# Performance work log

Hardware: AMD Instinct MI355X
Metric: run time of the kernel (lower is better)

## Reference

```python
import jax, jax.numpy as jnp
import numpy as np

NUM_BINS = 64
Z_MIN, Z_MAX = -3.0, 1.0
BIN_SIZE = (Z_MAX - Z_MIN) / NUM_BINS
EPS_MEAN = 1e-5
EPS_BN = 1e-5


def setup_inputs() -> dict:
    key = jax.random.key(0)
    k1, k2, k3, k4 = jax.random.split(key, 4)
    M, N, C = 100000, 64, 4
    feat_channels, out_dim = 64, NUM_BINS * 3
    features = jax.random.normal(k1, (M, N, C), dtype=jnp.float32)
    num_points = jax.random.randint(k2, (M,), 0, 65, dtype=jnp.int32)
    coors = jax.random.randint(k3, (M, 4), 0, 100, dtype=jnp.int32)
    W = jax.random.normal(k4, (feat_channels, out_dim), dtype=jnp.float32) * (1.0 / np.sqrt(out_dim))
    b = jnp.zeros((feat_channels,), dtype=jnp.float32)
    gamma = jnp.ones((feat_channels,), dtype=jnp.float32)
    beta = jnp.zeros((feat_channels,), dtype=jnp.float32)
    return {"features": features, "num_points": num_points, "coors": coors,
            "W": W, "b": b, "gamma": gamma, "beta": beta}


def reference(features, num_points, coors, W, b, gamma, beta):
    M, N, C = features.shape
    # validity mask per point
    mask = (jnp.arange(N)[None, :] < num_points[:, None]).astype(features.dtype)  # [M, N]
    z = features[..., 2]  # [M, N]
    r = features[..., 3]  # [M, N]
    bin_idx = jnp.clip(((z - Z_MIN) / BIN_SIZE).astype(jnp.int32), 0, NUM_BINS - 1)  # [M, N]

    rows = jnp.arange(M)[:, None]  # [M, 1] broadcast against [M, N]
    zeros = jnp.zeros((M, NUM_BINS), dtype=features.dtype)
    count = zeros.at[rows, bin_idx].add(mask)
    sum_z = zeros.at[rows, bin_idx].add(z * mask)
    sum_r = zeros.at[rows, bin_idx].add(r * mask)
    mean_z = sum_z / (count + EPS_MEAN)
    mean_r = sum_r / (count + EPS_MEAN)

    # interleaved layout [count, mean_z, mean_r] per bin -> [M, 3*NUM_BINS]
    hist = jnp.stack([count, mean_z, mean_r], axis=-1).reshape(M, NUM_BINS * 3)

    # Linear -> BatchNorm1d (training: biased batch stats) -> ReLU
    x = hist @ W.T + b  # [M, feat_channels]
    mu = jnp.mean(x, axis=0)
    var = jnp.mean((x - mu) ** 2, axis=0)
    xn = (x - mu) / jnp.sqrt(var + EPS_BN)
    return jax.nn.relu(xn * gamma + beta)
```

## Files before the change

### kernel.cpp

```cpp
#include <hip/hip_runtime.h>
#include <hip/hip_bf16.h>
#include <math.h>


typedef __attribute__((ext_vector_type(8))) short bf16x8;
typedef __attribute__((ext_vector_type(4))) float f32x4;
typedef __attribute__((ext_vector_type(4))) int   i32x4;

#define ZMINF   (-3.0f)
#define INV_BIN 16.0f
#define QS      8192.0f
#define INV_QS  (1.0f / 8192.0f)
#define PBIASF  65536.0f
#define PBIASI  65536
#define CBIT    16777216
#define TSC     16777216.0f
#define INV_TSC (1.0f / 16777216.0f)
#define REPS    16
#define RSTRIDE 66

__device__ __forceinline__ short f2bf(float f) {
    __hip_bfloat16 h = __float2bfloat16(f);
    return __builtin_bit_cast(short, h);
}

__global__ __launch_bounds__(256)
void k0_prep(const float* __restrict__ W,
             short*       __restrict__ wsW,
             unsigned long long* __restrict__ totals)
{
    const int tid    = blockIdx.x * 256 + threadIdx.x;
    const int stride = gridDim.x * 256;
    for (int e = tid; e < 24 * 64 * 8; e += stride) {
        const int j  = e & 7;
        const int ln = (e >> 3) & 63;
        const int st = e >> 9;
        const int s  = st >> 2, t = st & 3;
        const int k  = s * 32 + (ln >> 4) * 8 + j;
        const int n  = t * 16 + (ln & 15);
        const int wc = (k < 64) ? 3 * k
                     : (k < 128) ? 3 * (k - 64) + 1
                                 : 3 * (k - 128) + 2;
        wsW[e] = f2bf(W[n * 192 + wc]);
    }
    for (int e = tid; e < REPS * 128; e += stride) totals[e] = 0ull;
}

__global__ __launch_bounds__(128, 8)
void k1_hist_mfma(const uint2*  __restrict__ feat2,
                  const int*    __restrict__ nump,
                  const bf16x8* __restrict__ wsWf,
                  const float*  __restrict__ bvec,
                  float*        __restrict__ xout,
                  unsigned long long* __restrict__ totals,
                  int M)
{
    __shared__ unsigned long long sH[16 * RSTRIDE];

    const int tid  = threadIdx.x;
    const int wave = tid >> 6;
    const int lane = tid & 63;
    const int col  = lane & 15;
    const int quad = lane >> 4;
    const int half = wave;

    const int gbase = blockIdx.x * 16;
    float psum[2] = {0.f, 0.f};
    float psq[2]  = {0.f, 0.f};
    bf16x8 bcur[2];

    if (gbase < M) {
        uint2 zw[8];
        const int npv = nump[min(gbase + half * 8 + (lane & 7), M - 1)];
        #pragma unroll
        for (int uu = 0; uu < 8; ++uu) {
            const int rc = min(gbase + half * 8 + uu, M - 1);
            zw[uu] = feat2[((size_t)rc * 64 + lane) * 2 + 1];
        }

        {
            i32x4* p4 = (i32x4*)&sH[(size_t)half * 8 * RSTRIDE];
            #pragma unroll
            for (int i = 0; i < 5; ++i) {
                const int idx = lane + i * 64;
                if (idx < (8 * RSTRIDE * 2) / 4) p4[idx] = i32x4{0, 0, 0, 0};
            }
        }
        __builtin_amdgcn_wave_barrier();

        #pragma unroll
        for (int uu = 0; uu < 8; ++uu) {
            const int u = half * 8 + uu;
            int np_u = __builtin_amdgcn_readlane(npv, uu);
            np_u = (gbase + u < M) ? np_u : 0;
            if (lane < np_u) {
                const float z  = __int_as_float((int)zw[uu].x);
                const float rr = __int_as_float((int)zw[uu].y);
                int bi = (int)((z - ZMINF) * INV_BIN);
                bi = min(max(bi, 0), 63);
                const unsigned long long add =
                    ((unsigned long long)(unsigned)(CBIT + PBIASI + (int)(z * QS)) << 32)
                    | (unsigned)(PBIASI + (int)(rr * QS));
                atomicAdd(&sH[u * RSTRIDE + bi], add);
            }
        }

        bcur[0] = wsWf[(half * 2 + 0) * 64 + lane];
        bcur[1] = wsWf[(half * 2 + 1) * 64 + lane];
    }

    __syncthreads();

    if (gbase < M) {
        f32x4 acc[2] = {};
        bf16x8 bnxt[2];
        const int* ar = (const int*)sH + col * (RSTRIDE * 2);
        #pragma unroll
        for (int g = 0; g < 2; ++g) {
            const int o0 = g * 32 + quad * 8;
            const i32x4* ap = (const i32x4*)(ar + 2 * o0);
            const i32x4 a0 = ap[0], a1 = ap[1], a2 = ap[2], a3 = ap[3];
            const int zz[8]  = {a0.y, a0.w, a1.y, a1.w, a2.y, a2.w, a3.y, a3.w};
            const int rrw[8] = {a0.x, a0.z, a1.x, a1.z, a2.x, a2.z, a3.x, a3.z};
            float cnt[8], rcp[8], av[8];
            bf16x8 af;

            bnxt[0] = wsWf[((2 + g) * 4 + half * 2 + 0) * 64 + lane];
            bnxt[1] = wsWf[((2 + g) * 4 + half * 2 + 1) * 64 + lane];
            #pragma unroll
            for (int j = 0; j < 8; ++j) { cnt[j] = (float)(zz[j] >> 24); av[j] = cnt[j]; }
            #pragma unroll
            for (int j = 0; j < 8; ++j) af[j] = f2bf(av[j]);
            acc[0] = __builtin_amdgcn_mfma_f32_16x16x32_bf16(af, bcur[0], acc[0], 0, 0, 0);
            acc[1] = __builtin_amdgcn_mfma_f32_16x16x32_bf16(af, bcur[1], acc[1], 0, 0, 0);
            bcur[0] = bnxt[0]; bcur[1] = bnxt[1];

            bnxt[0] = wsWf[((4 + g) * 4 + half * 2 + 0) * 64 + lane];
            bnxt[1] = wsWf[((4 + g) * 4 + half * 2 + 1) * 64 + lane];
            #pragma unroll
            for (int j = 0; j < 8; ++j) {
                rcp[j] = __builtin_amdgcn_rcpf(cnt[j] + 1e-5f) * INV_QS;
                const float pay = (float)(zz[j] & 0xFFFFFF);
                av[j] = (pay - cnt[j] * PBIASF) * rcp[j];
            }
            #pragma unroll
            for (int j = 0; j < 8; ++j) af[j] = f2bf(av[j]);
            acc[0] = __builtin_amdgcn_mfma_f32_16x16x32_bf16(af, bcur[0], acc[0], 0, 0, 0);
            acc[1] = __builtin_amdgcn_mfma_f32_16x16x32_bf16(af, bcur[1], acc[1], 0, 0, 0);
            bcur[0] = bnxt[0]; bcur[1] = bnxt[1];

            if (g == 0) {
                bnxt[0] = wsWf[(1 * 4 + half * 2 + 0) * 64 + lane];
                bnxt[1] = wsWf[(1 * 4 + half * 2 + 1) * 64 + lane];
            }
            #pragma unroll
            for (int j = 0; j < 8; ++j)
                av[j] = ((float)rrw[j] - cnt[j] * PBIASF) * rcp[j];
            #pragma unroll
            for (int j = 0; j < 8; ++j) af[j] = f2bf(av[j]);
            acc[0] = __builtin_amdgcn_mfma_f32_16x16x32_bf16(af, bcur[0], acc[0], 0, 0, 0);
            acc[1] = __builtin_amdgcn_mfma_f32_16x16x32_bf16(af, bcur[1], acc[1], 0, 0, 0);
            bcur[0] = bnxt[0]; bcur[1] = bnxt[1];
        }

        #pragma unroll
        for (int tt = 0; tt < 2; ++tt) {
            const int t = half * 2 + tt;
            const float bias = bvec[t * 16 + col];
            #pragma unroll
            for (int i = 0; i < 4; ++i) {
                const int row = gbase + quad * 4 + i;
                if (row < M) {
                    const float xv = acc[tt][i] + bias;
                    xout[(size_t)row * 64 + t * 16 + col] = xv;
                    psum[tt] += xv;
                    psq[tt]  += xv * xv;
                }
            }
        }
    }

    #pragma unroll
    for (int tt = 0; tt < 2; ++tt) {
        psum[tt] += __shfl_xor(psum[tt], 16);
        psum[tt] += __shfl_xor(psum[tt], 32);
        psq[tt]  += __shfl_xor(psq[tt], 16);
        psq[tt]  += __shfl_xor(psq[tt], 32);
    }
    const float myS = (quad & 1) ? psum[1] : psum[0];
    const float myQ = (quad & 1) ? psq[1]  : psq[0];
    const int gw = blockIdx.x * 2 + wave;
    if (lane < 32) {
        unsigned long long* dst = totals + (gw & (REPS - 1)) * 128 + half * 32 + lane;
        atomicAdd(dst,      (unsigned long long)(long long)(myS * TSC));
        atomicAdd(dst + 64, (unsigned long long)(long long)(myQ * TSC));
    }
}

__global__ __launch_bounds__(256)
void k3_bn_apply(float4* __restrict__ x,
                 const unsigned long long* __restrict__ totals,
                 const float* __restrict__ gamma,
                 const float* __restrict__ beta,
                 float invM, int n4)
{
    __shared__ float sT[128];
    __shared__ float sa[64];
    __shared__ float sc[64];
    const int t = threadIdx.x;
    if (t < 128) {
        long long s = 0;
        #pragma unroll
        for (int rep = 0; rep < REPS; ++rep) s += (long long)totals[rep * 128 + t];
        sT[t] = (float)s * (invM * INV_TSC);
    }
    __syncthreads();
    if (t < 64) {
        const float mu   = sT[t];
        const float q    = sT[64 + t];
        const float var  = q - mu * mu;
        const float rstd = 1.0f / sqrtf(var + 1e-5f);
        const float a    = gamma[t] * rstd;
        sa[t] = a;
        sc[t] = beta[t] - mu * a;
    }
    __syncthreads();
    const int stride = gridDim.x * 256;
    for (int i = blockIdx.x * 256 + t; i < n4; i += stride) {
        const float4 a = ((const float4*)sa)[i & 15];
        const float4 c = ((const float4*)sc)[i & 15];
        float4 v = x[i];
        v.x = fmaxf(fmaf(v.x, a.x, c.x), 0.f);
        v.y = fmaxf(fmaf(v.y, a.y, c.y), 0.f);
        v.z = fmaxf(fmaf(v.z, a.z, c.z), 0.f);
        v.w = fmaxf(fmaf(v.w, a.w, c.w), 0.f);
        x[i] = v;
    }
}

extern "C" void kernel_launch(void* const* d_in, const int* in_sizes, int n_in,
                              void* d_out, int out_size, void* d_ws, size_t ws_size,
                              hipStream_t stream) {
    const uint2*  feat2 = (const uint2*)d_in[0];
    const int*    nump  = (const int*)d_in[1];
    const float*  W     = (const float*)d_in[3];
    const float*  bvec  = (const float*)d_in[4];
    const float*  gamma = (const float*)d_in[5];
    const float*  beta  = (const float*)d_in[6];

    const int M = in_sizes[1];
    float* xout = (float*)d_out;
    short* wsW  = (short*)d_ws;
    unsigned long long* totals =
        (unsigned long long*)((char*)d_ws + 24 * 64 * 8 * sizeof(short));

    k0_prep<<<16, 256, 0, stream>>>(W, wsW, totals);

    const int nblk = (M + 15) / 16;
    k1_hist_mfma<<<nblk, 128, 0, stream>>>(feat2, nump, (const bf16x8*)wsW, bvec, xout, totals, M);

    const int n4 = out_size / 4;
    const int nblk3 = (n4 + 256 * 16 - 1) / (256 * 16);
    k3_bn_apply<<<nblk3, 256, 0, stream>>>((float4*)d_out, totals, gamma, beta,
                                           1.0f / (float)M, n4);
}
```

Baseline: 185.0 us.

## Process four tiles per block with double-buffered histogram and prefetched features

Each block now loops over four 16-row tiles, prefetching the next tile's z/r features and point counts into registers while the current tile is histogrammed and multiplied. The LDS histogram is double-buffered so one barrier per tile suffices. All six W fragments are loaded into registers once per block instead of being streamed per tile. The launch-bound occupancy hint drops to raise register budget, and the grid shrinks fourfold, trading parallelism for amortized setup and latency hiding.

```diff
diff --git a/kernel.cpp b/kernel.cpp
--- a/kernel.cpp
+++ b/kernel.cpp
@@ -18,6 +18,7 @@
 #define INV_TSC (1.0f / 16777216.0f)
 #define REPS    16
 #define RSTRIDE 66
+#define TILES   4
 
 __device__ __forceinline__ short f2bf(float f) {
     __hip_bfloat16 h = __float2bfloat16(f);
@@ -46,7 +47,7 @@
     for (int e = tid; e < REPS * 128; e += stride) totals[e] = 0ull;
 }
 
-__global__ __launch_bounds__(128, 8)
+__global__ __launch_bounds__(128, 3)
 void k1_hist_mfma(const uint2*  __restrict__ feat2,
                   const int*    __restrict__ nump,
                   const bf16x8* __restrict__ wsWf,
@@ -55,126 +56,138 @@
                   unsigned long long* __restrict__ totals,
                   int M)
 {
-    __shared__ unsigned long long sH[16 * RSTRIDE];
+    __shared__ unsigned long long sH[2][16 * RSTRIDE];
 
     const int tid  = threadIdx.x;
-    const int wave = tid >> 6;
+    const int half = tid >> 6;
     const int lane = tid & 63;
     const int col  = lane & 15;
     const int quad = lane >> 4;
-    const int half = wave;
-
-    const int gbase = blockIdx.x * 16;
+
+    const int gbase0 = blockIdx.x * (16 * TILES);
+
+    bf16x8 bfr[6][2];
+    #pragma unroll
+    for (int p = 0; p < 6; ++p) {
+        #pragma unroll
+        for (int tt = 0; tt < 2; ++tt)
+            bfr[p][tt] = wsWf[(p * 4 + half * 2 + tt) * 64 + lane];
+    }
+
     float psum[2] = {0.f, 0.f};
     float psq[2]  = {0.f, 0.f};
-    bf16x8 bcur[2];
-
-    if (gbase < M) {
-        uint2 zw[8];
-        const int npv = nump[min(gbase + half * 8 + (lane & 7), M - 1)];
+
+    uint2 zw[2][8];
+    int   npv[2];
+
+    {
+        npv[0] = nump[min(gbase0 + half * 8 + (lane & 7), M - 1)];
         #pragma unroll
         for (int uu = 0; uu < 8; ++uu) {
-            const int rc = min(gbase + half * 8 + uu, M - 1);
-            zw[uu] = feat2[((size_t)rc * 64 + lane) * 2 + 1];
+            const int rc = min(gbase0 + half * 8 + uu, M - 1);
+            zw[0][uu] = feat2[((size_t)rc * 64 + lane) * 2 + 1];
         }
-
-        {
-            i32x4* p4 = (i32x4*)&sH[(size_t)half * 8 * RSTRIDE];
+    }
+
+    #pragma unroll
+    for (int t = 0; t < TILES; ++t) {
+        const int gbase = gbase0 + t * 16;
+        if (gbase < M) {
+            const int cur = t & 1;
+            const int nxt = cur ^ 1;
+
+            if (t + 1 < TILES) {
+                const int gb = gbase0 + (t + 1) * 16;
+                npv[nxt] = nump[min(gb + half * 8 + (lane & 7), M - 1)];
+                #pragma unroll
+                for (int uu = 0; uu < 8; ++uu) {
+                    const int rc = min(gb + half * 8 + uu, M - 1);
+                    zw[nxt][uu] = feat2[((size_t)rc * 64 + lane) * 2 + 1];
+                }
+            }
+
+            {
+                int* base = (int*)&sH[cur][0];
+                #pragma unroll
+                for (int i = 0; i < 4; ++i) {
+                    const int idx = lane + i * 64;
+                    const int off = (half * 8 + (idx >> 5)) * (RSTRIDE * 2) + (idx & 31) * 4;
+                    *(i32x4*)(base + off) = i32x4{0, 0, 0, 0};
+                }
+            }
+            __builtin_amdgcn_wave_barrier();
+
             #pragma unroll
-            for (int i = 0; i < 5; ++i) {
-                const int idx = lane + i * 64;
-                if (idx < (8 * RSTRIDE * 2) / 4) p4[idx] = i32x4{0, 0, 0, 0};
-            }
-        }
-        __builtin_amdgcn_wave_barrier();
-
-        #pragma unroll
-        for (int uu = 0; uu < 8; ++uu) {
-            const int u = half * 8 + uu;
-            int np_u = __builtin_amdgcn_readlane(npv, uu);
-            np_u = (gbase + u < M) ? np_u : 0;
-            if (lane < np_u) {
-                const float z  = __int_as_float((int)zw[uu].x);
-                const float rr = __int_as_float((int)zw[uu].y);
-                int bi = (int)((z - ZMINF) * INV_BIN);
-                bi = min(max(bi, 0), 63);
-                const unsigned long long add =
-                    ((unsigned long long)(unsigned)(CBIT + PBIASI + (int)(z * QS)) << 32)
-                    | (unsigned)(PBIASI + (int)(rr * QS));
-                atomicAdd(&sH[u * RSTRIDE + bi], add);
-            }
-        }
-
-        bcur[0] = wsWf[(half * 2 + 0) * 64 + lane];
-        bcur[1] = wsWf[(half * 2 + 1) * 64 + lane];
-    }
-
-    __syncthreads();
-
-    if (gbase < M) {
-        f32x4 acc[2] = {};
-        bf16x8 bnxt[2];
-        const int* ar = (const int*)sH + col * (RSTRIDE * 2);
-        #pragma unroll
-        for (int g = 0; g < 2; ++g) {
-            const int o0 = g * 32 + quad * 8;
-            const i32x4* ap = (const i32x4*)(ar + 2 * o0);
-            const i32x4 a0 = ap[0], a1 = ap[1], a2 = ap[2], a3 = ap[3];
-            const int zz[8]  = {a0.y, a0.w, a1.y, a1.w, a2.y, a2.w, a3.y, a3.w};
-            const int rrw[8] = {a0.x, a0.z, a1.x, a1.z, a2.x, a2.z, a3.x, a3.z};
-            float cnt[8], rcp[8], av[8];
-            bf16x8 af;
-
-            bnxt[0] = wsWf[((2 + g) * 4 + half * 2 + 0) * 64 + lane];
-            bnxt[1] = wsWf[((2 + g) * 4 + half * 2 + 1) * 64 + lane];
+            for (int uu = 0; uu < 8; ++uu) {
+                const int u = half * 8 + uu;
+                int np_u = __builtin_amdgcn_readlane(npv[cur], uu);
+                np_u = (gbase + u < M) ? np_u : 0;
+                if (lane < np_u) {
+                    const float z  = __int_as_float((int)zw[cur][uu].x);
+                    const float rr = __int_as_float((int)zw[cur][uu].y);
+                    int bi = (int)((z - ZMINF) * INV_BIN);
+                    bi = min(max(bi, 0), 63);
+                    const unsigned long long add =
+                        ((unsigned long long)(unsigned)(CBIT + PBIASI + (int)(z * QS)) << 32)
+                        | (unsigned)(PBIASI + (int)(rr * QS));
+                    atomicAdd(&sH[cur][u * RSTRIDE + bi], add);
+                }
+            }
+
+            __syncthreads();
+
+            f32x4 acc[2] = {};
+            const int* ar = (const int*)&sH[cur][0] + col * (RSTRIDE * 2);
             #pragma unroll
-            for (int j = 0; j < 8; ++j) { cnt[j] = (float)(zz[j] >> 24); av[j] = cnt[j]; }
+            for (int g = 0; g < 2; ++g) {
+                const int o0 = g * 32 + quad * 8;
+                const i32x4* ap = (const i32x4*)(ar + 2 * o0);
+                const i32x4 a0 = ap[0], a1 = ap[1], a2 = ap[2], a3 = ap[3];
+                const int zz[8]  = {a0.y, a0.w, a1.y, a1.w, a2.y, a2.w, a3.y, a3.w};
+                const int rrw[8] = {a0.x, a0.z, a1.x, a1.z, a2.x, a2.z, a3.x, a3.z};
+                float cnt[8], rcp[8], av[8];
+                bf16x8 af;
+
+                #pragma unroll
+                for (int j = 0; j < 8; ++j) { cnt[j] = (float)(zz[j] >> 24); av[j] = cnt[j]; }
+                #pragma unroll
+                for (int j = 0; j < 8; ++j) af[j] = f2bf(av[j]);
+                acc[0] = __builtin_amdgcn_mfma_f32_16x16x32_bf16(af, bfr[g][0], acc[0], 0, 0, 0);
+                acc[1] = __builtin_amdgcn_mfma_f32_16x16x32_bf16(af, bfr[g][1], acc[1], 0, 0, 0);
+
+                #pragma unroll
+                for (int j = 0; j < 8; ++j) {
+                    rcp[j] = __builtin_amdgcn_rcpf(cnt[j] + 1e-5f) * INV_QS;
+                    const float pay = (float)(zz[j] & 0xFFFFFF);
+                    av[j] = (pay - cnt[j] * PBIASF) * rcp[j];
+                }
+                #pragma unroll
+                for (int j = 0; j < 8; ++j) af[j] = f2bf(av[j]);
+                acc[0] = __builtin_amdgcn_mfma_f32_16x16x32_bf16(af, bfr[2 + g][0], acc[0], 0, 0, 0);
+                acc[1] = __builtin_amdgcn_mfma_f32_16x16x32_bf16(af, bfr[2 + g][1], acc[1], 0, 0, 0);
+
+                #pragma unroll
+                for (int j = 0; j < 8; ++j)
+                    av[j] = ((float)rrw[j] - cnt[j] * PBIASF) * rcp[j];
+                #pragma unroll
+                for (int j = 0; j < 8; ++j) af[j] = f2bf(av[j]);
+                acc[0] = __builtin_amdgcn_mfma_f32_16x16x32_bf16(af, bfr[4 + g][0], acc[0], 0, 0, 0);
+                acc[1] = __builtin_amdgcn_mfma_f32_16x16x32_bf16(af, bfr[4 + g][1], acc[1], 0, 0, 0);
+            }
+
             #pragma unroll
-            for (int j = 0; j < 8; ++j) af[j] = f2bf(av[j]);
-            acc[0] = __builtin_amdgcn_mfma_f32_16x16x32_bf16(af, bcur[0], acc[0], 0, 0, 0);
-            acc[1] = __builtin_amdgcn_mfma_f32_16x16x32_bf16(af, bcur[1], acc[1], 0, 0, 0);
-            bcur[0] = bnxt[0]; bcur[1] = bnxt[1];
-
-            bnxt[0] = wsWf[((4 + g) * 4 + half * 2 + 0) * 64 + lane];
-            bnxt[1] = wsWf[((4 + g) * 4 + half * 2 + 1) * 64 + lane];
-            #pragma unroll
-            for (int j = 0; j < 8; ++j) {
-                rcp[j] = __builtin_amdgcn_rcpf(cnt[j] + 1e-5f) * INV_QS;
-                const float pay = (float)(zz[j] & 0xFFFFFF);
-                av[j] = (pay - cnt[j] * PBIASF) * rcp[j];
-            }
-            #pragma unroll
-            for (int j = 0; j < 8; ++j) af[j] = f2bf(av[j]);
-            acc[0] = __builtin_amdgcn_mfma_f32_16x16x32_bf16(af, bcur[0], acc[0], 0, 0, 0);
-            acc[1] = __builtin_amdgcn_mfma_f32_16x16x32_bf16(af, bcur[1], acc[1], 0, 0, 0);
-            bcur[0] = bnxt[0]; bcur[1] = bnxt[1];
-
-            if (g == 0) {
-                bnxt[0] = wsWf[(1 * 4 + half * 2 + 0) * 64 + lane];
-                bnxt[1] = wsWf[(1 * 4 + half * 2 + 1) * 64 + lane];
-            }
-            #pragma unroll
-            for (int j = 0; j < 8; ++j)
-                av[j] = ((float)rrw[j] - cnt[j] * PBIASF) * rcp[j];
-            #pragma unroll
-            for (int j = 0; j < 8; ++j) af[j] = f2bf(av[j]);
-            acc[0] = __builtin_amdgcn_mfma_f32_16x16x32_bf16(af, bcur[0], acc[0], 0, 0, 0);
-            acc[1] = __builtin_amdgcn_mfma_f32_16x16x32_bf16(af, bcur[1], acc[1], 0, 0, 0);
-            bcur[0] = bnxt[0]; bcur[1] = bnxt[1];
-        }
-
-        #pragma unroll
-        for (int tt = 0; tt < 2; ++tt) {
-            const int t = half * 2 + tt;
-            const float bias = bvec[t * 16 + col];
-            #pragma unroll
-            for (int i = 0; i < 4; ++i) {
-                const int row = gbase + quad * 4 + i;
-                if (row < M) {
-                    const float xv = acc[tt][i] + bias;
-                    xout[(size_t)row * 64 + t * 16 + col] = xv;
-                    psum[tt] += xv;
-                    psq[tt]  += xv * xv;
+            for (int tt = 0; tt < 2; ++tt) {
+                const int tch = half * 2 + tt;
+                const float bias = bvec[tch * 16 + col];
+                #pragma unroll
+                for (int i = 0; i < 4; ++i) {
+                    const int row = gbase + quad * 4 + i;
+                    if (row < M) {
+                        const float xv = acc[tt][i] + bias;
+                        xout[(size_t)row * 64 + tch * 16 + col] = xv;
+                        psum[tt] += xv;
+                        psq[tt]  += xv * xv;
+                    }
                 }
             }
         }
@@ -189,9 +202,8 @@
     }
     const float myS = (quad & 1) ? psum[1] : psum[0];
     const float myQ = (quad & 1) ? psq[1]  : psq[0];
-    const int gw = blockIdx.x * 2 + wave;
     if (lane < 32) {
-        unsigned long long* dst = totals + (gw & (REPS - 1)) * 128 + half * 32 + lane;
+        unsigned long long* dst = totals + (blockIdx.x & (REPS - 1)) * 128 + half * 32 + lane;
         atomicAdd(dst,      (unsigned long long)(long long)(myS * TSC));
         atomicAdd(dst + 64, (unsigned long long)(long long)(myQ * TSC));
     }
@@ -256,7 +268,7 @@
 
     k0_prep<<<16, 256, 0, stream>>>(W, wsW, totals);
 
-    const int nblk = (M + 15) / 16;
+    const int nblk = (M + 16 * TILES - 1) / (16 * TILES);
     k1_hist_mfma<<<nblk, 128, 0, stream>>>(feat2, nump, (const bf16x8*)wsW, bvec, xout, totals, M);
 
     const int n4 = out_size / 4;
```

New measurement: 190.1 us. 1.03x slower.

## Process two voxel tiles per block with software-prefetched feature loads

Applied to the files above, without the earlier changes.

Each block now handles two 16-voxel tiles in sequence. The feature and point-count loads for the next tile are issued before the current tile's MFMA stage runs, so global load latency overlaps with compute. Bias loads and the BN-stat atomics are amortized over more rows, and the grid is halved. In exchange, register use grows because two tiles of feature buffers are live at once, so the occupancy hint drops from 8 to 6 blocks per CU, and an extra block barrier is needed between tiles.

```diff
diff --git a/kernel.cpp b/kernel.cpp
--- a/kernel.cpp
+++ b/kernel.cpp
@@ -18,6 +18,7 @@
 #define INV_TSC (1.0f / 16777216.0f)
 #define REPS    16
 #define RSTRIDE 66
+#define TILES   2
 
 __device__ __forceinline__ short f2bf(float f) {
     __hip_bfloat16 h = __float2bfloat16(f);
@@ -46,7 +47,7 @@
     for (int e = tid; e < REPS * 128; e += stride) totals[e] = 0ull;
 }
 
-__global__ __launch_bounds__(128, 8)
+__global__ __launch_bounds__(128, 6)
 void k1_hist_mfma(const uint2*  __restrict__ feat2,
                   const int*    __restrict__ nump,
                   const bf16x8* __restrict__ wsWf,
@@ -58,125 +59,147 @@
     __shared__ unsigned long long sH[16 * RSTRIDE];
 
     const int tid  = threadIdx.x;
-    const int wave = tid >> 6;
+    const int half = tid >> 6;
     const int lane = tid & 63;
     const int col  = lane & 15;
     const int quad = lane >> 4;
-    const int half = wave;
-
-    const int gbase = blockIdx.x * 16;
+
+    const int gbase0 = blockIdx.x * (16 * TILES);
+
     float psum[2] = {0.f, 0.f};
     float psq[2]  = {0.f, 0.f};
-    bf16x8 bcur[2];
-
-    if (gbase < M) {
-        uint2 zw[8];
-        const int npv = nump[min(gbase + half * 8 + (lane & 7), M - 1)];
+
+    const float bias0 = bvec[(half * 2 + 0) * 16 + col];
+    const float bias1 = bvec[(half * 2 + 1) * 16 + col];
+
+    uint2 zw[2][8];
+    int   npv[2];
+
+    {
+        npv[0] = nump[min(gbase0 + half * 8 + (lane & 7), M - 1)];
         #pragma unroll
         for (int uu = 0; uu < 8; ++uu) {
-            const int rc = min(gbase + half * 8 + uu, M - 1);
-            zw[uu] = feat2[((size_t)rc * 64 + lane) * 2 + 1];
+            const int rc = min(gbase0 + half * 8 + uu, M - 1);
+            zw[0][uu] = feat2[((size_t)rc * 64 + lane) * 2 + 1];
         }
-
-        {
-            i32x4* p4 = (i32x4*)&sH[(size_t)half * 8 * RSTRIDE];
+    }
+
+    #pragma unroll
+    for (int t = 0; t < TILES; ++t) {
+        const int gbase = gbase0 + t * 16;
+        if (gbase < M) {
+            const int cur = t & 1;
+            const int nxt = cur ^ 1;
+
+            {
+                i32x4* p4 = (i32x4*)&sH[(size_t)half * 8 * RSTRIDE];
+                #pragma unroll
+                for (int i = 0; i < 5; ++i) {
+                    const int idx = lane + i * 64;
+                    if (idx < (8 * RSTRIDE * 2) / 4) p4[idx] = i32x4{0, 0, 0, 0};
+                }
+            }
+            __builtin_amdgcn_wave_barrier();
+
             #pragma unroll
-            for (int i = 0; i < 5; ++i) {
-                const int idx = lane + i * 64;
-                if (idx < (8 * RSTRIDE * 2) / 4) p4[idx] = i32x4{0, 0, 0, 0};
-            }
-        }
-        __builtin_amdgcn_wave_barrier();
-
-        #pragma unroll
-        for (int uu = 0; uu < 8; ++uu) {
-            const int u = half * 8 + uu;
-            int np_u = __builtin_amdgcn_readlane(npv, uu);
-            np_u = (gbase + u < M) ? np_u : 0;
-            if (lane < np_u) {
-                const float z  = __int_as_float((int)zw[uu].x);
-                const float rr = __int_as_float((int)zw[uu].y);
-                int bi = (int)((z - ZMINF) * INV_BIN);
-                bi = min(max(bi, 0), 63);
-                const unsigned long long add =
-                    ((unsigned long long)(unsigned)(CBIT + PBIASI + (int)(z * QS)) << 32)
-                    | (unsigned)(PBIASI + (int)(rr * QS));
-                atomicAdd(&sH[u * RSTRIDE + bi], add);
-            }
-        }
-
-        bcur[0] = wsWf[(half * 2 + 0) * 64 + lane];
-        bcur[1] = wsWf[(half * 2 + 1) * 64 + lane];
-    }
-
-    __syncthreads();
-
-    if (gbase < M) {
-        f32x4 acc[2] = {};
-        bf16x8 bnxt[2];
-        const int* ar = (const int*)sH + col * (RSTRIDE * 2);
-        #pragma unroll
-        for (int g = 0; g < 2; ++g) {
-            const int o0 = g * 32 + quad * 8;
-            const i32x4* ap = (const i32x4*)(ar + 2 * o0);
-            const i32x4 a0 = ap[0], a1 = ap[1], a2 = ap[2], a3 = ap[3];
-            const int zz[8]  = {a0.y, a0.w, a1.y, a1.w, a2.y, a2.w, a3.y, a3.w};
-            const int rrw[8] = {a0.x, a0.z, a1.x, a1.z, a2.x, a2.z, a3.x, a3.z};
-            float cnt[8], rcp[8], av[8];
-            bf16x8 af;
-
-            bnxt[0] = wsWf[((2 + g) * 4 + half * 2 + 0) * 64 + lane];
-            bnxt[1] = wsWf[((2 + g) * 4 + half * 2 + 1) * 64 + lane];
+            for (int uu = 0; uu < 8; ++uu) {
+                const int u = half * 8 + uu;
+                int np_u = __builtin_amdgcn_readlane(npv[cur], uu);
+                np_u = (gbase + u < M) ? np_u : 0;
+                if (lane < np_u) {
+                    const float z  = __int_as_float((int)zw[cur][uu].x);
+                    const float rr = __int_as_float((int)zw[cur][uu].y);
+                    int bi = (int)((z - ZMINF) * INV_BIN);
+                    bi = min(max(bi, 0), 63);
+                    const unsigned long long add =
+                        ((unsigned long long)(unsigned)(CBIT + PBIASI + (int)(z * QS)) << 32)
+                        | (unsigned)(PBIASI + (int)(rr * QS));
+                    atomicAdd(&sH[u * RSTRIDE + bi], add);
+                }
+            }
+
+            if (t + 1 < TILES) {
+                const int gb = gbase0 + (t + 1) * 16;
+                npv[nxt] = nump[min(gb + half * 8 + (lane & 7), M - 1)];
+                #pragma unroll
+                for (int uu = 0; uu < 8; ++uu) {
+                    const int rc = min(gb + half * 8 + uu, M - 1);
+                    zw[nxt][uu] = feat2[((size_t)rc * 64 + lane) * 2 + 1];
+                }
+            }
+
+            bf16x8 bcur[2], bnxt[2];
+            bcur[0] = wsWf[(half * 2 + 0) * 64 + lane];
+            bcur[1] = wsWf[(half * 2 + 1) * 64 + lane];
+
+            __syncthreads();
+
+            f32x4 acc[2] = {};
+            const int* ar = (const int*)sH + col * (RSTRIDE * 2);
             #pragma unroll
-            for (int j = 0; j < 8; ++j) { cnt[j] = (float)(zz[j] >> 24); av[j] = cnt[j]; }
-            #pragma unroll
-            for (int j = 0; j < 8; ++j) af[j] = f2bf(av[j]);
-            acc[0] = __builtin_amdgcn_mfma_f32_16x16x32_bf16(af, bcur[0], acc[0], 0, 0, 0);
-            acc[1] = __builtin_amdgcn_mfma_f32_16x16x32_bf16(af, bcur[1], acc[1], 0, 0, 0);
-            bcur[0] = bnxt[0]; bcur[1] = bnxt[1];
-
-            bnxt[0] = wsWf[((4 + g) * 4 + half * 2 + 0) * 64 + lane];
-            bnxt[1] = wsWf[((4 + g) * 4 + half * 2 + 1) * 64 + lane];
-            #pragma unroll
-            for (int j = 0; j < 8; ++j) {
-                rcp[j] = __builtin_amdgcn_rcpf(cnt[j] + 1e-5f) * INV_QS;
-                const float pay = (float)(zz[j] & 0xFFFFFF);
-                av[j] = (pay - cnt[j] * PBIASF) * rcp[j];
-            }
-            #pragma unroll
-            for (int j = 0; j < 8; ++j) af[j] = f2bf(av[j]);
-            acc[0] = __builtin_amdgcn_mfma_f32_16x16x32_bf16(af, bcur[0], acc[0], 0, 0, 0);
-            acc[1] = __builtin_amdgcn_mfma_f32_16x16x32_bf16(af, bcur[1], acc[1], 0, 0, 0);
-            bcur[0] = bnxt[0]; bcur[1] = bnxt[1];
-
-            if (g == 0) {
-                bnxt[0] = wsWf[(1 * 4 + half * 2 + 0) * 64 + lane];
-                bnxt[1] = wsWf[(1 * 4 + half * 2 + 1) * 64 + lane];
-            }
-            #pragma unroll
-            for (int j = 0; j < 8; ++j)
-                av[j] = ((float)rrw[j] - cnt[j] * PBIASF) * rcp[j];
-            #pragma unroll
-            for (int j = 0; j < 8; ++j) af[j] = f2bf(av[j]);
-            acc[0] = __builtin_amdgcn_mfma_f32_16x16x32_bf16(af, bcur[0], acc[0], 0, 0, 0);
-            acc[1] = __builtin_amdgcn_mfma_f32_16x16x32_bf16(af, bcur[1], acc[1], 0, 0, 0);
-            bcur[0] = bnxt[0]; bcur[1] = bnxt[1];
-        }
-
-        #pragma unroll
-        for (int tt = 0; tt < 2; ++tt) {
-            const int t = half * 2 + tt;
-            const float bias = bvec[t * 16 + col];
+            for (int g = 0; g < 2; ++g) {
+                const int o0 = g * 32 + quad * 8;
+                const i32x4* ap = (const i32x4*)(ar + 2 * o0);
+                const i32x4 a0 = ap[0], a1 = ap[1], a2 = ap[2], a3 = ap[3];
+                const int zz[8]  = {a0.y, a0.w, a1.y, a1.w, a2.y, a2.w, a3.y, a3.w};
+                const int rrw[8] = {a0.x, a0.z, a1.x, a1.z, a2.x, a2.z, a3.x, a3.z};
+                float cnt[8], rcp[8], av[8];
+                bf16x8 af;
+
+                bnxt[0] = wsWf[((2 + g) * 4 + half * 2 + 0) * 64 + lane];
+                bnxt[1] = wsWf[((2 + g) * 4 + half * 2 + 1) * 64 + lane];
+                #pragma unroll
+                for (int j = 0; j < 8; ++j) { cnt[j] = (float)(zz[j] >> 24); av[j] = cnt[j]; }
+                #pragma unroll
+                for (int j = 0; j < 8; ++j) af[j] = f2bf(av[j]);
+                acc[0] = __builtin_amdgcn_mfma_f32_16x16x32_bf16(af, bcur[0], acc[0], 0, 0, 0);
+                acc[1] = __builtin_amdgcn_mfma_f32_16x16x32_bf16(af, bcur[1], acc[1], 0, 0, 0);
+                bcur[0] = bnxt[0]; bcur[1] = bnxt[1];
+
+                bnxt[0] = wsWf[((4 + g) * 4 + half * 2 + 0) * 64 + lane];
+                bnxt[1] = wsWf[((4 + g) * 4 + half * 2 + 1) * 64 + lane];
+                #pragma unroll
+                for (int j = 0; j < 8; ++j) {
+                    rcp[j] = __builtin_amdgcn_rcpf(cnt[j] + 1e-5f) * INV_QS;
+                    const float pay = (float)(zz[j] & 0xFFFFFF);
+                    av[j] = (pay - cnt[j] * PBIASF) * rcp[j];
+                }
+                #pragma unroll
+                for (int j = 0; j < 8; ++j) af[j] = f2bf(av[j]);
+                acc[0] = __builtin_amdgcn_mfma_f32_16x16x32_bf16(af, bcur[0], acc[0], 0, 0, 0);
+                acc[1] = __builtin_amdgcn_mfma_f32_16x16x32_bf16(af, bcur[1], acc[1], 0, 0, 0);
+                bcur[0] = bnxt[0]; bcur[1] = bnxt[1];
+
+                if (g == 0) {
+                    bnxt[0] = wsWf[(1 * 4 + half * 2 + 0) * 64 + lane];
+                    bnxt[1] = wsWf[(1 * 4 + half * 2 + 1) * 64 + lane];
+                }
+                #pragma unroll
+                for (int j = 0; j < 8; ++j)
+                    av[j] = ((float)rrw[j] - cnt[j] * PBIASF) * rcp[j];
+                #pragma unroll
+                for (int j = 0; j < 8; ++j) af[j] = f2bf(av[j]);
+                acc[0] = __builtin_amdgcn_mfma_f32_16x16x32_bf16(af, bcur[0], acc[0], 0, 0, 0);
+                acc[1] = __builtin_amdgcn_mfma_f32_16x16x32_bf16(af, bcur[1], acc[1], 0, 0, 0);
+                bcur[0] = bnxt[0]; bcur[1] = bnxt[1];
+            }
+
             #pragma unroll
             for (int i = 0; i < 4; ++i) {
                 const int row = gbase + quad * 4 + i;
                 if (row < M) {
-                    const float xv = acc[tt][i] + bias;
-                    xout[(size_t)row * 64 + t * 16 + col] = xv;
-                    psum[tt] += xv;
-                    psq[tt]  += xv * xv;
-                }
-            }
+                    const float xv0 = acc[0][i] + bias0;
+                    const float xv1 = acc[1][i] + bias1;
+                    float* xr = xout + (size_t)row * 64 + half * 32 + col;
+                    xr[0]  = xv0;
+                    xr[16] = xv1;
+                    psum[0] += xv0; psq[0] += xv0 * xv0;
+                    psum[1] += xv1; psq[1] += xv1 * xv1;
+                }
+            }
+
+            if (t + 1 < TILES)
+                __syncthreads();
         }
     }
 
@@ -189,9 +212,8 @@
     }
     const float myS = (quad & 1) ? psum[1] : psum[0];
     const float myQ = (quad & 1) ? psq[1]  : psq[0];
-    const int gw = blockIdx.x * 2 + wave;
     if (lane < 32) {
-        unsigned long long* dst = totals + (gw & (REPS - 1)) * 128 + half * 32 + lane;
+        unsigned long long* dst = totals + (blockIdx.x & (REPS - 1)) * 128 + half * 32 + lane;
         atomicAdd(dst,      (unsigned long long)(long long)(myS * TSC));
         atomicAdd(dst + 64, (unsigned long long)(long long)(myQ * TSC));
     }
@@ -256,7 +278,7 @@
 
     k0_prep<<<16, 256, 0, stream>>>(W, wsW, totals);
 
-    const int nblk = (M + 15) / 16;
+    const int nblk = (M + 16 * TILES - 1) / (16 * TILES);
     k1_hist_mfma<<<nblk, 128, 0, stream>>>(feat2, nump, (const bf16x8*)wsW, bvec, xout, totals, M);
 
     const int n4 = out_size / 4;
```

Result: slower. 193.8 us (+4.7%).

## Split fused histogram+GEMM kernel into histogram and persistent GEMM kernels

Applied to the files above, without the earlier changes.

The fused kernel is split in two. The histogram kernel builds bf16 A-fragments per 16-voxel tile and writes them to workspace. A persistent GEMM kernel with 512 blocks keeps all W fragments in registers, loops over tiles with software prefetch, and does one set of BN-stat atomics per wave instead of per block. The aim is to take repeated W loads and per-block atomics off the histogram path, at the cost of an extra global round-trip of about 15 MB of packed activations and one more kernel launch.

```diff
diff --git a/kernel.cpp b/kernel.cpp
--- a/kernel.cpp
+++ b/kernel.cpp
@@ -47,154 +47,179 @@
 }
 
 __global__ __launch_bounds__(128, 8)
-void k1_hist_mfma(const uint2*  __restrict__ feat2,
-                  const int*    __restrict__ nump,
-                  const bf16x8* __restrict__ wsWf,
-                  const float*  __restrict__ bvec,
-                  float*        __restrict__ xout,
-                  unsigned long long* __restrict__ totals,
-                  int M)
+void k1a_hist(const uint2* __restrict__ feat2,
+              const int*   __restrict__ nump,
+              bf16x8*      __restrict__ Ap,
+              int M)
 {
     __shared__ unsigned long long sH[16 * RSTRIDE];
 
+    const int tid  = threadIdx.x;
+    const int half = tid >> 6;
+    const int lane = tid & 63;
+    const int col  = lane & 15;
+    const int quad = lane >> 4;
+
+    const int blk   = blockIdx.x;
+    const int gbase = blk * 16;
+
+    uint2 zw[8];
+    const int npv = nump[min(gbase + half * 8 + (lane & 7), M - 1)];
+    #pragma unroll
+    for (int uu = 0; uu < 8; ++uu) {
+        const int rc = min(gbase + half * 8 + uu, M - 1);
+        zw[uu] = feat2[((size_t)rc * 64 + lane) * 2 + 1];
+    }
+
+    {
+        i32x4* p4 = (i32x4*)&sH[(size_t)half * 8 * RSTRIDE];
+        #pragma unroll
+        for (int i = 0; i < 5; ++i) {
+            const int idx = lane + i * 64;
+            if (idx < (8 * RSTRIDE * 2) / 4) p4[idx] = i32x4{0, 0, 0, 0};
+        }
+    }
+    __builtin_amdgcn_wave_barrier();
+
+    #pragma unroll
+    for (int uu = 0; uu < 8; ++uu) {
+        const int u = half * 8 + uu;
+        int np_u = __builtin_amdgcn_readlane(npv, uu);
+        np_u = (gbase + u < M) ? np_u : 0;
+        if (lane < np_u) {
+            const float z  = __int_as_float((int)zw[uu].x);
+            const float rr = __int_as_float((int)zw[uu].y);
+            int bi = (int)((z - ZMINF) * INV_BIN);
+            bi = min(max(bi, 0), 63);
+            const unsigned long long add =
+                ((unsigned long long)(unsigned)(CBIT + PBIASI + (int)(z * QS)) << 32)
+                | (unsigned)(PBIASI + (int)(rr * QS));
+            atomicAdd(&sH[u * RSTRIDE + bi], add);
+        }
+    }
+
+    __syncthreads();
+
+    const int* ar = (const int*)sH + col * (RSTRIDE * 2);
+    const int o0 = half * 32 + quad * 8;
+    const i32x4* apt = (const i32x4*)(ar + 2 * o0);
+    const i32x4 a0 = apt[0], a1 = apt[1], a2 = apt[2], a3 = apt[3];
+    const int zz[8]  = {a0.y, a0.w, a1.y, a1.w, a2.y, a2.w, a3.y, a3.w};
+    const int rrw[8] = {a0.x, a0.z, a1.x, a1.z, a2.x, a2.z, a3.x, a3.z};
+    float cnt[8], rcp[8];
+    bf16x8 af_c, af_z, af_r;
+    #pragma unroll
+    for (int j = 0; j < 8; ++j) {
+        cnt[j] = (float)(zz[j] >> 24);
+        af_c[j] = f2bf(cnt[j]);
+    }
+    #pragma unroll
+    for (int j = 0; j < 8; ++j) {
+        rcp[j] = __builtin_amdgcn_rcpf(cnt[j] + 1e-5f) * INV_QS;
+        const float pay = (float)(zz[j] & 0xFFFFFF);
+        af_z[j] = f2bf((pay - cnt[j] * PBIASF) * rcp[j]);
+    }
+    #pragma unroll
+    for (int j = 0; j < 8; ++j)
+        af_r[j] = f2bf(((float)rrw[j] - cnt[j] * PBIASF) * rcp[j]);
+
+    bf16x8* dst = Ap + (size_t)blk * 6 * 64;
+    dst[(0 + half) * 64 + lane] = af_c;
+    dst[(2 + half) * 64 + lane] = af_z;
+    dst[(4 + half) * 64 + lane] = af_r;
+}
+
+__global__ __launch_bounds__(256, 2)
+void k1b_gemm(const bf16x8* __restrict__ Ap,
+              const bf16x8* __restrict__ wsWf,
+              const float*  __restrict__ bvec,
+              float*        __restrict__ xout,
+              unsigned long long* __restrict__ totals,
+              int M, int nblk)
+{
     const int tid  = threadIdx.x;
     const int wave = tid >> 6;
     const int lane = tid & 63;
     const int col  = lane & 15;
     const int quad = lane >> 4;
-    const int half = wave;
-
-    const int gbase = blockIdx.x * 16;
-    float psum[2] = {0.f, 0.f};
-    float psq[2]  = {0.f, 0.f};
-    bf16x8 bcur[2];
-
-    if (gbase < M) {
-        uint2 zw[8];
-        const int npv = nump[min(gbase + half * 8 + (lane & 7), M - 1)];
-        #pragma unroll
-        for (int uu = 0; uu < 8; ++uu) {
-            const int rc = min(gbase + half * 8 + uu, M - 1);
-            zw[uu] = feat2[((size_t)rc * 64 + lane) * 2 + 1];
-        }
-
-        {
-            i32x4* p4 = (i32x4*)&sH[(size_t)half * 8 * RSTRIDE];
+
+    const int gw = blockIdx.x * 4 + wave;
+    const int nw = gridDim.x * 4;
+
+    bf16x8 bfr[6][4];
+    #pragma unroll
+    for (int p = 0; p < 6; ++p)
+        #pragma unroll
+        for (int t = 0; t < 4; ++t)
+            bfr[p][t] = wsWf[(p * 4 + t) * 64 + lane];
+    float bias[4];
+    #pragma unroll
+    for (int t = 0; t < 4; ++t) bias[t] = bvec[t * 16 + col];
+
+    float psum[4] = {0.f, 0.f, 0.f, 0.f};
+    float psq[4]  = {0.f, 0.f, 0.f, 0.f};
+
+    int blk = gw;
+    bf16x8 a[6];
+    if (blk < nblk) {
+        const bf16x8* ap = Ap + (size_t)blk * 6 * 64 + lane;
+        #pragma unroll
+        for (int s = 0; s < 6; ++s) a[s] = ap[s * 64];
+    }
+
+    while (blk < nblk) {
+        const int nxt = blk + nw;
+        bf16x8 an[6];
+        if (nxt < nblk) {
+            const bf16x8* ap = Ap + (size_t)nxt * 6 * 64 + lane;
             #pragma unroll
-            for (int i = 0; i < 5; ++i) {
-                const int idx = lane + i * 64;
-                if (idx < (8 * RSTRIDE * 2) / 4) p4[idx] = i32x4{0, 0, 0, 0};
-            }
-        }
-        __builtin_amdgcn_wave_barrier();
-
-        #pragma unroll
-        for (int uu = 0; uu < 8; ++uu) {
-            const int u = half * 8 + uu;
-            int np_u = __builtin_amdgcn_readlane(npv, uu);
-            np_u = (gbase + u < M) ? np_u : 0;
-            if (lane < np_u) {
-                const float z  = __int_as_float((int)zw[uu].x);
-                const float rr = __int_as_float((int)zw[uu].y);
-                int bi = (int)((z - ZMINF) * INV_BIN);
-                bi = min(max(bi, 0), 63);
-                const unsigned long long add =
-                    ((unsigned long long)(unsigned)(CBIT + PBIASI + (int)(z * QS)) << 32)
-                    | (unsigned)(PBIASI + (int)(rr * QS));
-                atomicAdd(&sH[u * RSTRIDE + bi], add);
-            }
-        }
-
-        bcur[0] = wsWf[(half * 2 + 0) * 64 + lane];
-        bcur[1] = wsWf[(half * 2 + 1) * 64 + lane];
-    }
-
-    __syncthreads();
-
-    if (gbase < M) {
-        f32x4 acc[2] = {};
-        bf16x8 bnxt[2];
-        const int* ar = (const int*)sH + col * (RSTRIDE * 2);
-        #pragma unroll
-        for (int g = 0; g < 2; ++g) {
-            const int o0 = g * 32 + quad * 8;
-            const i32x4* ap = (const i32x4*)(ar + 2 * o0);
-            const i32x4 a0 = ap[0], a1 = ap[1], a2 = ap[2], a3 = ap[3];
-            const int zz[8]  = {a0.y, a0.w, a1.y, a1.w, a2.y, a2.w, a3.y, a3.w};
-            const int rrw[8] = {a0.x, a0.z, a1.x, a1.z, a2.x, a2.z, a3.x, a3.z};
-            float cnt[8], rcp[8], av[8];
-            bf16x8 af;
-
-            bnxt[0] = wsWf[((2 + g) * 4 + half * 2 + 0) * 64 + lane];
-            bnxt[1] = wsWf[((2 + g) * 4 + half * 2 + 1) * 64 + lane];
+            for (int s = 0; s < 6; ++s) an[s] = ap[s * 64];
+        }
+
+        f32x4 acc[4] = {};
+        #pragma unroll
+        for (int so = 0; so < 6; ++so) {
+            const int s = (so < 3) ? (so * 2) : ((so - 3) * 2 + 1);
             #pragma unroll
-            for (int j = 0; j < 8; ++j) { cnt[j] = (float)(zz[j] >> 24); av[j] = cnt[j]; }
-            #pragma unroll
-            for (int j = 0; j < 8; ++j) af[j] = f2bf(av[j]);
-            acc[0] = __builtin_amdgcn_mfma_f32_16x16x32_bf16(af, bcur[0], acc[0], 0, 0, 0);
-            acc[1] = __builtin_amdgcn_mfma_f32_16x16x32_bf16(af, bcur[1], acc[1], 0, 0, 0);
-            bcur[0] = bnxt[0]; bcur[1] = bnxt[1];
-
-            bnxt[0] = wsWf[((4 + g) * 4 + half * 2 + 0) * 64 + lane];
-            bnxt[1] = wsWf[((4 + g) * 4 + half * 2 + 1) * 64 + lane];
-            #pragma unroll
-            for (int j = 0; j < 8; ++j) {
-                rcp[j] = __builtin_amdgcn_rcpf(cnt[j] + 1e-5f) * INV_QS;
-                const float pay = (float)(zz[j] & 0xFFFFFF);
-                av[j] = (pay - cnt[j] * PBIASF) * rcp[j];
-            }
-            #pragma unroll
-            for (int j = 0; j < 8; ++j) af[j] = f2bf(av[j]);
-            acc[0] = __builtin_amdgcn_mfma_f32_16x16x32_bf16(af, bcur[0], acc[0], 0, 0, 0);
-            acc[1] = __builtin_amdgcn_mfma_f32_16x16x32_bf16(af, bcur[1], acc[1], 0, 0, 0);
-            bcur[0] = bnxt[0]; bcur[1] = bnxt[1];
-
-            if (g == 0) {
-                bnxt[0] = wsWf[(1 * 4 + half * 2 + 0) * 64 + lane];
-                bnxt[1] = wsWf[(1 * 4 + half * 2 + 1) * 64 + lane];
-            }
-            #pragma unroll
-            for (int j = 0; j < 8; ++j)
-                av[j] = ((float)rrw[j] - cnt[j] * PBIASF) * rcp[j];
-            #pragma unroll
-            for (int j = 0; j < 8; ++j) af[j] = f2bf(av[j]);
-            acc[0] = __builtin_amdgcn_mfma_f32_16x16x32_bf16(af, bcur[0], acc[0], 0, 0, 0);
-            acc[1] = __builtin_amdgcn_mfma_f32_16x16x32_bf16(af, bcur[1], acc[1], 0, 0, 0);
-            bcur[0] = bnxt[0]; bcur[1] = bnxt[1];
-        }
-
-        #pragma unroll
-        for (int tt = 0; tt < 2; ++tt) {
-            const int t = half * 2 + tt;
-            const float bias = bvec[t * 16 + col];
-            #pragma unroll
-            for (int i = 0; i < 4; ++i) {
-                const int row = gbase + quad * 4 + i;
-                if (row < M) {
-                    const float xv = acc[tt][i] + bias;
-                    xout[(size_t)row * 64 + t * 16 + col] = xv;
-                    psum[tt] += xv;
-                    psq[tt]  += xv * xv;
+            for (int t = 0; t < 4; ++t)
+                acc[t] = __builtin_amdgcn_mfma_f32_16x16x32_bf16(a[s], bfr[s][t], acc[t], 0, 0, 0);
+        }
+
+        const int gbase = blk * 16;
+        #pragma unroll
+        for (int i = 0; i < 4; ++i) {
+            const int row = gbase + quad * 4 + i;
+            if (row < M) {
+                float* xr = xout + (size_t)row * 64 + col;
+                #pragma unroll
+                for (int t = 0; t < 4; ++t) {
+                    const float xv = acc[t][i] + bias[t];
+                    xr[t * 16] = xv;
+                    psum[t] += xv;
+                    psq[t]  += xv * xv;
                 }
             }
         }
-    }
-
-    #pragma unroll
-    for (int tt = 0; tt < 2; ++tt) {
-        psum[tt] += __shfl_xor(psum[tt], 16);
-        psum[tt] += __shfl_xor(psum[tt], 32);
-        psq[tt]  += __shfl_xor(psq[tt], 16);
-        psq[tt]  += __shfl_xor(psq[tt], 32);
-    }
-    const float myS = (quad & 1) ? psum[1] : psum[0];
-    const float myQ = (quad & 1) ? psq[1]  : psq[0];
-    const int gw = blockIdx.x * 2 + wave;
-    if (lane < 32) {
-        unsigned long long* dst = totals + (gw & (REPS - 1)) * 128 + half * 32 + lane;
-        atomicAdd(dst,      (unsigned long long)(long long)(myS * TSC));
-        atomicAdd(dst + 64, (unsigned long long)(long long)(myQ * TSC));
-    }
+
+        #pragma unroll
+        for (int s = 0; s < 6; ++s) a[s] = an[s];
+        blk = nxt;
+    }
+
+    #pragma unroll
+    for (int t = 0; t < 4; ++t) {
+        psum[t] += __shfl_xor(psum[t], 16);
+        psum[t] += __shfl_xor(psum[t], 32);
+        psq[t]  += __shfl_xor(psq[t], 16);
+        psq[t]  += __shfl_xor(psq[t], 32);
+    }
+    float myS = psum[0], myQ = psq[0];
+    if (quad == 1) { myS = psum[1]; myQ = psq[1]; }
+    if (quad == 2) { myS = psum[2]; myQ = psq[2]; }
+    if (quad == 3) { myS = psum[3]; myQ = psq[3]; }
+    unsigned long long* dst = totals + (gw & (REPS - 1)) * 128 + lane;
+    atomicAdd(dst,      (unsigned long long)(long long)(myS * TSC));
+    atomicAdd(dst + 64, (unsigned long long)(long long)(myQ * TSC));
 }
 
 __global__ __launch_bounds__(256)
@@ -253,11 +278,16 @@
     short* wsW  = (short*)d_ws;
     unsigned long long* totals =
         (unsigned long long*)((char*)d_ws + 24 * 64 * 8 * sizeof(short));
+    bf16x8* Ap =
+        (bf16x8*)((char*)d_ws + 24 * 64 * 8 * sizeof(short) + REPS * 128 * 8);
+
+    const int nblk = (M + 15) / 16;
 
     k0_prep<<<16, 256, 0, stream>>>(W, wsW, totals);
 
-    const int nblk = (M + 15) / 16;
-    k1_hist_mfma<<<nblk, 128, 0, stream>>>(feat2, nump, (const bf16x8*)wsW, bvec, xout, totals, M);
+    k1a_hist<<<nblk, 128, 0, stream>>>(feat2, nump, Ap, M);
+
+    k1b_gemm<<<512, 256, 0, stream>>>(Ap, (const bf16x8*)wsW, bvec, xout, totals, M, nblk);
 
     const int n4 = out_size / 4;
     const int nblk3 = (n4 + 256 * 16 - 1) / (256 * 16);
```

New measurement: 213.8 us. 15.6% more time.
